# Performance work log

Measured on AMD Instinct MI355X. Metric: run time of the kernel, lower is better.

## Reference

```python
import jax, jax.numpy as jnp
import numpy as np

B, N, E, H = 32, 1024, 1024, 8
D = E // H      # head_dim = 128, att_mid_dim = [128, 64, 128]
MID = 64


def setup_inputs() -> dict:
    key = jax.random.key(0)
    ks = jax.random.split(key, 12)

    def lin(k, out_d, in_d):
        return (jax.random.normal(k, (out_d, in_d), jnp.float32) * 0.02,
                jnp.zeros((out_d,), jnp.float32))

    Wq, bq = lin(ks[0], E, E)
    Wk, bk = lin(ks[1], E, E)
    Wv, bv = lin(ks[2], E, E)
    Wb, bb = lin(ks[3], MID, D)    # attention_basic: Linear(mid[0]=D -> mid[1]=64) + ReLU
    Wl, bl = lin(ks[4], 1, MID)    # attention_last: Linear(64 -> 1)
    Wl2, bl2 = lin(ks[5], D, MID)  # attention_last2: Linear(64 -> D)
    query = jax.random.normal(ks[6], (B, E), jnp.float32)
    k_in = jax.random.normal(ks[7], (B, N, E), jnp.float32)
    value1 = jax.random.normal(ks[8], (B, E), jnp.float32)
    value2 = jax.random.normal(ks[9], (B, N, E), jnp.float32)
    mask = jax.random.randint(ks[10], (B, N), 0, 2, jnp.int32)
    mask = mask.at[:, 0].set(1)  # guarantee at least one valid position per row
    return {"query": query, "key": k_in, "mask": mask, "value1": value1,
            "value2": value2, "Wq": Wq, "bq": bq, "Wk": Wk, "bk": bk,
            "Wv": Wv, "bv": bv, "Wb": Wb, "bb": bb, "Wl": Wl, "bl": bl,
            "Wl2": Wl2, "bl2": bl2}


def reference(query, key, mask, value1, value2, Wq, bq, Wk, bk, Wv, bv,
              Wb, bb, Wl, bl, Wl2, bl2):
    # --- QKV projections (single-query attention) ---
    Q = (query @ Wq.T + bq).reshape(B, 1, H, D).transpose(0, 2, 1, 3)    # [B,H,1,D]
    K = (key @ Wk.T + bk).reshape(B, N, H, D).transpose(0, 2, 1, 3)      # [B,H,N,D]
    V = (key @ Wv.T + bv).reshape(B, N, H, D).transpose(0, 2, 1, 3)      # [B,H,N,D]
    v1 = value1.reshape(B, H, D)                                          # [B,H,D]
    v2 = (value2 @ Wv.T + bv).reshape(B, N, H, D).transpose(0, 2, 1, 3)   # [B,H,N,D]

    scores = jnp.einsum('bhqd,bhkd->bhqk', Q, K) / jnp.sqrt(jnp.float32(D))  # [B,H,1,N]
    attended = jnp.einsum('bhqk,bhkd->bhqd', scores, V)                      # [B,H,1,D]
    attn_map = jnp.broadcast_to(attended, (B, H, N, D))                      # expand(-1,-1,N,-1)

    # --- SCAtt attn_net ---
    h = jax.nn.relu(jnp.einsum('bhnd,md->bhnm', attn_map, Wb) + bb)          # [B,H,N,64]
    mf = mask.astype(h.dtype)                                                # [B,N]
    mext = mf[:, None, :, None]                                              # [B,1,N,1]
    att_map_pool = jnp.sum(h * mext, axis=2) / jnp.sum(mext, axis=2)         # [B,H,64]
    alpha_spatial = (jnp.einsum('bhnm,om->bhno', h, Wl) + bl)[..., 0]        # [B,H,N]
    alpha_channel = jax.nn.sigmoid(att_map_pool @ Wl2.T + bl2)               # [B,H,D]
    alpha_spatial = jnp.where(mf[:, None, :] == 0, jnp.float32(-1e9), alpha_spatial)
    alpha_spatial = jax.nn.softmax(alpha_spatial, axis=-1)                   # [B,H,N]
    v2_att = jnp.einsum('bhn,bhnd->bhd', alpha_spatial, v2)                  # [B,H,D]
    attn = v1 * v2_att * alpha_channel                                       # [B,H,D]
    return attn.reshape(B, H * D)
```

## Files before the change

kernel.cpp:

```cpp
#include <hip/hip_runtime.h>

#define B_  32
#define N_  1024
#define E_  1024
#define H_  8
#define D_  128
#define MID_ 64
#define NT_  16
#define TR_  64
#define NS2_ 16


__global__ __launch_bounds__(256) void k_pre(
        const float* __restrict__ query, const float* __restrict__ Wq,
        const float* __restrict__ bq, const float* __restrict__ Wk,
        const float* __restrict__ bk, float* __restrict__ qk,
        float* __restrict__ qb,
        const float* __restrict__ value2, const int* __restrict__ mask,
        float* __restrict__ P2)
{
    const int t = threadIdx.x;

    __shared__ float Qp[2][D_];
    __shared__ float Qs[D_];
    __shared__ float red[2];
    __shared__ int rows[N_ / NS2_];
    __shared__ int nrows;

    if (blockIdx.x < 256) {
        const int bh = blockIdx.x;
        const int b = bh >> 3, h = bh & 7;

        {
            const int d = t & 127, half = t >> 7;
            const int row = h * D_ + d;
            const float4* wr = (const float4*)(Wq + (size_t)row * E_) + half * 128;
            const float4* qr = (const float4*)(query + (size_t)b * E_) + half * 128;
            float acc = 0.f;
            #pragma unroll 8
            for (int i = 0; i < 128; ++i) {
                float4 w = wr[i], q = qr[i];
                acc += w.x * q.x + w.y * q.y + w.z * q.z + w.w * q.w;
            }
            Qp[half][d] = acc;
        }
        __syncthreads();
        if (t < D_) {
            const int row = h * D_ + t;
            float q = Qp[0][t] + Qp[1][t] + bq[row];
            Qs[t] = q;
            float qp = q * bk[row];
            #pragma unroll
            for (int off = 32; off; off >>= 1) qp += __shfl_down(qp, off);
            if ((t & 63) == 0) red[t >> 6] = qp;
        }
        __syncthreads();
        if (t == 0) qb[bh] = red[0] + red[1];

        const int e0 = t * 4;
        float4 a = make_float4(0.f, 0.f, 0.f, 0.f);
        const float* wkb = Wk + (size_t)(h * D_) * E_ + e0;
        #pragma unroll 8
        for (int d = 0; d < D_; ++d) {
            float Qd = Qs[d];
            float4 w = *(const float4*)(wkb + (size_t)d * E_);
            a.x += Qd * w.x; a.y += Qd * w.y; a.z += Qd * w.z; a.w += Qd * w.w;
        }
        *(float4*)(qk + (size_t)bh * E_ + e0) = a;
    } else {
        const int idx = blockIdx.x - 256;
        const int b = idx & 31, ns = idx >> 5;
        const int e0 = t * 4;
        const int n0 = ns * (N_ / NS2_);

        if (t == 0) nrows = 0;
        __syncthreads();
        if (t < N_ / NS2_) {
            if (mask[b * N_ + n0 + t]) {
                int i2 = atomicAdd(&nrows, 1);
                rows[i2] = t;
            }
        }
        __syncthreads();
        const int nr = nrows;

        float a0 = 0.f, a1 = 0.f, a2 = 0.f, a3 = 0.f;
        const float* vb = value2 + ((size_t)(b * N_ + n0)) * E_ + e0;
        #pragma unroll 4
        for (int i = 0; i < nr; ++i) {
            float4 v = *(const float4*)(vb + (size_t)rows[i] * E_);
            a0 += v.x; a1 += v.y; a2 += v.z; a3 += v.w;
        }
        float* dst = P2 + (size_t)b * E_ + e0;
        atomicAdd(dst + 0, a0); atomicAdd(dst + 1, a1);
        atomicAdd(dst + 2, a2); atomicAdd(dst + 3, a3);
    }
}

__global__ __launch_bounds__(256) void k_scorepool(
        const float* __restrict__ key, const float* __restrict__ qk,
        const float* __restrict__ qb, float* __restrict__ PP,
        float* __restrict__ ssum)
{
    const int tile = blockIdx.x, b = blockIdx.y;
    const int t = threadIdx.x;
    const int c = t & 31, g = t >> 5;

    __shared__ __align__(16) float qks[H_ * E_];
    __shared__ __align__(16) float ssc[TR_][H_];

    {
        const float4* src = (const float4*)(qk + (size_t)b * H_ * E_);
        float4* dst = (float4*)qks;
        #pragma unroll
        for (int k = 0; k < 8; ++k) dst[t + k * 256] = src[t + k * 256];
    }
    __syncthreads();

    const float scale = 0.08838834764831845f;
    const float* keyb = key + ((size_t)b * N_ + (size_t)tile * TR_) * E_;
    const float4* qks4 = (const float4*)qks;
    const float qbv = qb[b * 8 + (c & 7)];

    float acc[H_][8];
    #pragma unroll
    for (int h = 0; h < H_; ++h)
        #pragma unroll
        for (int j = 0; j < 8; ++j) acc[h][j] = 0.f;

    const float4* kr[8];
    #pragma unroll
    for (int j = 0; j < 8; ++j)
        kr[j] = (const float4*)(keyb + (size_t)(g * 8 + j) * E_);

    #pragma unroll 2
    for (int i = 0; i < 8; ++i) {
        float4 kf[8];
        #pragma unroll
        for (int j = 0; j < 8; ++j) kf[j] = kr[j][i * 32 + c];
        #pragma unroll
        for (int h = 0; h < H_; ++h) {
            float4 qf = qks4[h * 256 + i * 32 + c];
            #pragma unroll
            for (int j = 0; j < 8; ++j) {
                acc[h][j] += qf.x * kf[j].x + qf.y * kf[j].y
                           + qf.z * kf[j].z + qf.w * kf[j].w;
            }
        }
    }
    #pragma unroll
    for (int off = 16; off; off >>= 1) {
        #pragma unroll
        for (int h = 0; h < H_; ++h)
            #pragma unroll
            for (int j = 0; j < 8; ++j)
                acc[h][j] += __shfl_xor(acc[h][j], off);
    }
    float tsum = 0.f;
    #pragma unroll
    for (int h = 0; h < H_; ++h) {
        if (c == h) {
            #pragma unroll
            for (int j = 0; j < 8; ++j) {
                float s = (acc[h][j] + qbv) * scale;
                ssc[g * 8 + j][h] = s;
                tsum += s;
            }
        }
    }
    if (c < H_) atomicAdd(&ssum[b * 8 + c], tsum);
    __syncthreads();

    {
        const int e0 = t * 4;
        float pacc[H_][4] = {};
        const float* kb = keyb + e0;
        #pragma unroll 4
        for (int n = 0; n < TR_; ++n) {
            float4 kv = *(const float4*)(kb + (size_t)n * E_);
            float4 s0 = *(const float4*)&ssc[n][0];
            float4 s1 = *(const float4*)&ssc[n][4];
            pacc[0][0] += s0.x * kv.x; pacc[0][1] += s0.x * kv.y;
            pacc[0][2] += s0.x * kv.z; pacc[0][3] += s0.x * kv.w;
            pacc[1][0] += s0.y * kv.x; pacc[1][1] += s0.y * kv.y;
            pacc[1][2] += s0.y * kv.z; pacc[1][3] += s0.y * kv.w;
            pacc[2][0] += s0.z * kv.x; pacc[2][1] += s0.z * kv.y;
            pacc[2][2] += s0.z * kv.z; pacc[2][3] += s0.z * kv.w;
            pacc[3][0] += s0.w * kv.x; pacc[3][1] += s0.w * kv.y;
            pacc[3][2] += s0.w * kv.z; pacc[3][3] += s0.w * kv.w;
            pacc[4][0] += s1.x * kv.x; pacc[4][1] += s1.x * kv.y;
            pacc[4][2] += s1.x * kv.z; pacc[4][3] += s1.x * kv.w;
            pacc[5][0] += s1.y * kv.x; pacc[5][1] += s1.y * kv.y;
            pacc[5][2] += s1.y * kv.z; pacc[5][3] += s1.y * kv.w;
            pacc[6][0] += s1.z * kv.x; pacc[6][1] += s1.z * kv.y;
            pacc[6][2] += s1.z * kv.z; pacc[6][3] += s1.z * kv.w;
            pacc[7][0] += s1.w * kv.x; pacc[7][1] += s1.w * kv.y;
            pacc[7][2] += s1.w * kv.z; pacc[7][3] += s1.w * kv.w;
        }
        #pragma unroll
        for (int h = 0; h < H_; ++h) {
            float* dst = PP + ((size_t)(b * H_) + h) * E_ + e0;
            atomicAdd(dst + 0, pacc[h][0]); atomicAdd(dst + 1, pacc[h][1]);
            atomicAdd(dst + 2, pacc[h][2]); atomicAdd(dst + 3, pacc[h][3]);
        }
    }
}

__global__ __launch_bounds__(256) void k_final(
        const float* __restrict__ PP, const float* __restrict__ P2,
        const float* __restrict__ ssumg, const int* __restrict__ mask,
        const float* __restrict__ Wv, const float* __restrict__ bv,
        const float* __restrict__ Wb, const float* __restrict__ bb,
        const float* __restrict__ Wl2, const float* __restrict__ bl2,
        const float* __restrict__ value1, float* __restrict__ out)
{
    const int bh = blockIdx.x, b = bh >> 3, h = bh & 7;
    const int t = threadIdx.x;
    const int l = t & 63, w = t >> 6;
    const int rg = l >> 4, cl = l & 15;

    __shared__ __align__(16) float pooled[E_];
    __shared__ __align__(16) float pool2[E_];
    __shared__ float attA_s[D_];
    __shared__ float attV_s[D_];
    __shared__ float att[D_];
    __shared__ float hv[MID_];
    __shared__ float red2[4];
    __shared__ float cnt_s;

    {
        const float4* pp = (const float4*)(PP + ((size_t)(b * H_) + h) * E_);
        const float4* p2 = (const float4*)(P2 + (size_t)b * E_);
        ((float4*)pooled)[t] = pp[t];
        ((float4*)pool2)[t]  = p2[t];

        int ci = 0;
        #pragma unroll
        for (int i = 0; i < 4; ++i) ci += mask[b * N_ + t + i * 256];
        float cf = (float)ci;
        #pragma unroll
        for (int off = 32; off; off >>= 1) cf += __shfl_down(cf, off);
        if (l == 0) red2[w] = cf;
    }
    __syncthreads();
    if (t == 0) cnt_s = red2[0] + red2[1] + red2[2] + red2[3];

    const float4* pooled4 = (const float4*)pooled;
    const float4* pool24  = (const float4*)pool2;
    #pragma unroll 2
    for (int pass = 0; pass < 8; ++pass) {
        const int d = pass * 16 + w * 4 + rg;
        const float4* wvr = (const float4*)(Wv + (size_t)(h * D_ + d) * E_);
        float pA = 0.f, pV = 0.f;
        #pragma unroll 4
        for (int i = 0; i < 16; ++i) {
            float4 wv4 = wvr[cl + i * 16];
            float4 pa = pooled4[cl + i * 16];
            float4 pb = pool24[cl + i * 16];
            pA += wv4.x * pa.x + wv4.y * pa.y + wv4.z * pa.z + wv4.w * pa.w;
            pV += wv4.x * pb.x + wv4.y * pb.y + wv4.z * pb.z + wv4.w * pb.w;
        }
        #pragma unroll
        for (int off = 8; off; off >>= 1) {
            pA += __shfl_xor(pA, off);
            pV += __shfl_xor(pV, off);
        }
        if (cl == 0) { attA_s[d] = pA; attV_s[d] = pV; }
    }
    __syncthreads();
    const float cnt = cnt_s;
    const float ss = ssumg[bh];
    if (t < D_) att[t] = attA_s[t] + ss * bv[h * D_ + t];
    __syncthreads();
    if (t < MID_) {
        float a = bb[t];
        #pragma unroll 4
        for (int d2 = 0; d2 < D_; ++d2) a += att[d2] * Wb[t * D_ + d2];
        hv[t] = fmaxf(a, 0.f);
    }
    __syncthreads();
    if (t < D_) {
        float z = bl2[t];
        #pragma unroll
        for (int m = 0; m < MID_; ++m) z += hv[m] * Wl2[t * MID_ + m];
        float alphac = 1.f / (1.f + expf(-z));
        const float bvd = bv[h * D_ + t];
        float v2a = attV_s[t] / cnt + bvd;
        out[(size_t)b * E_ + h * D_ + t] =
            value1[(size_t)b * E_ + h * D_ + t] * v2a * alphac;
    }
}

extern "C" void kernel_launch(void* const* d_in, const int* in_sizes, int n_in,
                              void* d_out, int out_size, void* d_ws, size_t ws_size,
                              hipStream_t stream)
{
    const float* query  = (const float*)d_in[0];
    const float* key    = (const float*)d_in[1];
    const int*   mask   = (const int*)d_in[2];
    const float* value1 = (const float*)d_in[3];
    const float* value2 = (const float*)d_in[4];
    const float* Wq  = (const float*)d_in[5];
    const float* bq  = (const float*)d_in[6];
    const float* Wk  = (const float*)d_in[7];
    const float* bk  = (const float*)d_in[8];
    const float* Wv  = (const float*)d_in[9];
    const float* bv  = (const float*)d_in[10];
    const float* Wb  = (const float*)d_in[11];
    const float* bb  = (const float*)d_in[12];
    const float* Wl2 = (const float*)d_in[15];
    const float* bl2 = (const float*)d_in[16];
    float* out = (float*)d_out;

    char* ws = (char*)d_ws;
    const size_t OFF_P2 = (size_t)B_ * H_ * E_ * 4;
    const size_t OFF_SS = OFF_P2 + (size_t)B_ * E_ * 4;
    const size_t OFF_QB = OFF_SS + 1024;
    const size_t OFF_QK = OFF_QB + 1024;
    float* PP   = (float*)(ws);
    float* P2   = (float*)(ws + OFF_P2);
    float* ssum = (float*)(ws + OFF_SS);
    float* qb   = (float*)(ws + OFF_QB);
    float* qk   = (float*)(ws + OFF_QK);

    hipMemsetAsync(d_ws, 0, OFF_QB, stream);

    hipLaunchKernelGGL(k_pre, dim3(256 + NS2_ * B_), dim3(256), 0, stream,
                       query, Wq, bq, Wk, bk, qk, qb, value2, mask, P2);
    hipLaunchKernelGGL(k_scorepool, dim3(NT_, B_), dim3(256), 0, stream,
                       key, qk, qb, PP, ssum);
    hipLaunchKernelGGL(k_final, dim3(B_ * H_), dim3(256), 0, stream,
                       PP, P2, ssum, mask, Wv, bv, Wb, bb, Wl2, bl2, value1, out);
}
```

Baseline: 427.0 us.

## Split score/pool and Wv projection across more blocks; coalesce Q projection

The Q projection in k_pre now stages the query row in shared memory and uses 16-lane groups with shuffle reductions, so Wq rows are read coalesced. k_scorepool splits the 8 heads into two groups of 4, which doubles the grid and halves per-thread accumulators. The Wv projection moves into a new k_att kernel spread over 4 blocks per (b,h), and a small k_final handles the tail. The aim is more parallelism and occupancy, at the cost of reading key twice and adding one more kernel launch.

New measurement: 443.1 us. 3.8% more time.

```diff
diff --git a/kernel.cpp b/kernel.cpp
--- a/kernel.cpp
+++ b/kernel.cpp
@@ -21,41 +21,48 @@
 {
     const int t = threadIdx.x;
 
-    __shared__ float Qp[2][D_];
+    __shared__ __align__(16) float qsh[E_];
     __shared__ float Qs[D_];
-    __shared__ float red[2];
+    __shared__ float red[4];
     __shared__ int rows[N_ / NS2_];
     __shared__ int nrows;
 
     if (blockIdx.x < 256) {
         const int bh = blockIdx.x;
         const int b = bh >> 3, h = bh & 7;
-
-        {
-            const int d = t & 127, half = t >> 7;
+        const int l = t & 63, w = t >> 6;
+        const int rg = l >> 4, cl = l & 15;
+
+        ((float4*)qsh)[t] = ((const float4*)(query + (size_t)b * E_))[t];
+        __syncthreads();
+
+        const float4* qsh4 = (const float4*)qsh;
+        float qbacc = 0.f;
+        #pragma unroll 2
+        for (int p = 0; p < 8; ++p) {
+            const int d = p * 16 + w * 4 + rg;
             const int row = h * D_ + d;
-            const float4* wr = (const float4*)(Wq + (size_t)row * E_) + half * 128;
-            const float4* qr = (const float4*)(query + (size_t)b * E_) + half * 128;
+            const float4* wr = (const float4*)(Wq + (size_t)row * E_);
             float acc = 0.f;
-            #pragma unroll 8
-            for (int i = 0; i < 128; ++i) {
-                float4 w = wr[i], q = qr[i];
-                acc += w.x * q.x + w.y * q.y + w.z * q.z + w.w * q.w;
-            }
-            Qp[half][d] = acc;
-        }
+            #pragma unroll 4
+            for (int i = 0; i < 16; ++i) {
+                float4 wv = wr[cl + i * 16];
+                float4 qv = qsh4[cl + i * 16];
+                acc += wv.x * qv.x + wv.y * qv.y + wv.z * qv.z + wv.w * qv.w;
+            }
+            #pragma unroll
+            for (int off = 8; off; off >>= 1) acc += __shfl_xor(acc, off);
+            if (cl == 0) {
+                float q = acc + bq[row];
+                Qs[d] = q;
+                qbacc += q * bk[row];
+            }
+        }
+        #pragma unroll
+        for (int off = 32; off; off >>= 1) qbacc += __shfl_down(qbacc, off);
+        if (l == 0) red[w] = qbacc;
         __syncthreads();
-        if (t < D_) {
-            const int row = h * D_ + t;
-            float q = Qp[0][t] + Qp[1][t] + bq[row];
-            Qs[t] = q;
-            float qp = q * bk[row];
-            #pragma unroll
-            for (int off = 32; off; off >>= 1) qp += __shfl_down(qp, off);
-            if ((t & 63) == 0) red[t >> 6] = qp;
-        }
-        __syncthreads();
-        if (t == 0) qb[bh] = red[0] + red[1];
+        if (t == 0) qb[bh] = red[0] + red[1] + red[2] + red[3];
 
         const int e0 = t * 4;
         float4 a = make_float4(0.f, 0.f, 0.f, 0.f);
@@ -63,8 +70,8 @@
         #pragma unroll 8
         for (int d = 0; d < D_; ++d) {
             float Qd = Qs[d];
-            float4 w = *(const float4*)(wkb + (size_t)d * E_);
-            a.x += Qd * w.x; a.y += Qd * w.y; a.z += Qd * w.z; a.w += Qd * w.w;
+            float4 wv = *(const float4*)(wkb + (size_t)d * E_);
+            a.x += Qd * wv.x; a.y += Qd * wv.y; a.z += Qd * wv.z; a.w += Qd * wv.w;
         }
         *(float4*)(qk + (size_t)bh * E_ + e0) = a;
     } else {
@@ -102,31 +109,32 @@
         const float* __restrict__ qb, float* __restrict__ PP,
         float* __restrict__ ssum)
 {
-    const int tile = blockIdx.x, b = blockIdx.y;
+    const int hh = blockIdx.x;
+    const int tile = blockIdx.y, b = blockIdx.z;
     const int t = threadIdx.x;
     const int c = t & 31, g = t >> 5;
 
-    __shared__ __align__(16) float qks[H_ * E_];
-    __shared__ __align__(16) float ssc[TR_][H_];
+    __shared__ __align__(16) float qks[4 * E_];
+    __shared__ __align__(16) float ssc[TR_][4];
 
     {
-        const float4* src = (const float4*)(qk + (size_t)b * H_ * E_);
+        const float4* src = (const float4*)(qk + ((size_t)b * H_ + hh * 4) * E_);
         float4* dst = (float4*)qks;
         #pragma unroll
-        for (int k = 0; k < 8; ++k) dst[t + k * 256] = src[t + k * 256];
+        for (int k = 0; k < 4; ++k) dst[t + k * 256] = src[t + k * 256];
     }
     __syncthreads();
 
     const float scale = 0.08838834764831845f;
     const float* keyb = key + ((size_t)b * N_ + (size_t)tile * TR_) * E_;
     const float4* qks4 = (const float4*)qks;
-    const float qbv = qb[b * 8 + (c & 7)];
-
-    float acc[H_][8];
-    #pragma unroll
-    for (int h = 0; h < H_; ++h)
-        #pragma unroll
-        for (int j = 0; j < 8; ++j) acc[h][j] = 0.f;
+    const float qbv = qb[b * 8 + hh * 4 + (c & 3)];
+
+    float acc[4][8];
+    #pragma unroll
+    for (int lh = 0; lh < 4; ++lh)
+        #pragma unroll
+        for (int j = 0; j < 8; ++j) acc[lh][j] = 0.f;
 
     const float4* kr[8];
     #pragma unroll
@@ -139,117 +147,87 @@
         #pragma unroll
         for (int j = 0; j < 8; ++j) kf[j] = kr[j][i * 32 + c];
         #pragma unroll
-        for (int h = 0; h < H_; ++h) {
-            float4 qf = qks4[h * 256 + i * 32 + c];
+        for (int lh = 0; lh < 4; ++lh) {
+            float4 qf = qks4[lh * 256 + i * 32 + c];
             #pragma unroll
             for (int j = 0; j < 8; ++j) {
-                acc[h][j] += qf.x * kf[j].x + qf.y * kf[j].y
-                           + qf.z * kf[j].z + qf.w * kf[j].w;
+                acc[lh][j] += qf.x * kf[j].x + qf.y * kf[j].y
+                            + qf.z * kf[j].z + qf.w * kf[j].w;
             }
         }
     }
     #pragma unroll
     for (int off = 16; off; off >>= 1) {
         #pragma unroll
-        for (int h = 0; h < H_; ++h)
+        for (int lh = 0; lh < 4; ++lh)
             #pragma unroll
             for (int j = 0; j < 8; ++j)
-                acc[h][j] += __shfl_xor(acc[h][j], off);
+                acc[lh][j] += __shfl_xor(acc[lh][j], off);
     }
     float tsum = 0.f;
     #pragma unroll
-    for (int h = 0; h < H_; ++h) {
-        if (c == h) {
+    for (int lh = 0; lh < 4; ++lh) {
+        if (c == lh) {
             #pragma unroll
             for (int j = 0; j < 8; ++j) {
-                float s = (acc[h][j] + qbv) * scale;
-                ssc[g * 8 + j][h] = s;
+                float s = (acc[lh][j] + qbv) * scale;
+                ssc[g * 8 + j][lh] = s;
                 tsum += s;
             }
         }
     }
-    if (c < H_) atomicAdd(&ssum[b * 8 + c], tsum);
+    if (c < 4) atomicAdd(&ssum[b * 8 + hh * 4 + c], tsum);
     __syncthreads();
 
     {
         const int e0 = t * 4;
-        float pacc[H_][4] = {};
+        float pacc[4][4] = {};
         const float* kb = keyb + e0;
         #pragma unroll 4
         for (int n = 0; n < TR_; ++n) {
             float4 kv = *(const float4*)(kb + (size_t)n * E_);
-            float4 s0 = *(const float4*)&ssc[n][0];
-            float4 s1 = *(const float4*)&ssc[n][4];
-            pacc[0][0] += s0.x * kv.x; pacc[0][1] += s0.x * kv.y;
-            pacc[0][2] += s0.x * kv.z; pacc[0][3] += s0.x * kv.w;
-            pacc[1][0] += s0.y * kv.x; pacc[1][1] += s0.y * kv.y;
-            pacc[1][2] += s0.y * kv.z; pacc[1][3] += s0.y * kv.w;
-            pacc[2][0] += s0.z * kv.x; pacc[2][1] += s0.z * kv.y;
-            pacc[2][2] += s0.z * kv.z; pacc[2][3] += s0.z * kv.w;
-            pacc[3][0] += s0.w * kv.x; pacc[3][1] += s0.w * kv.y;
-            pacc[3][2] += s0.w * kv.z; pacc[3][3] += s0.w * kv.w;
-            pacc[4][0] += s1.x * kv.x; pacc[4][1] += s1.x * kv.y;
-            pacc[4][2] += s1.x * kv.z; pacc[4][3] += s1.x * kv.w;
-            pacc[5][0] += s1.y * kv.x; pacc[5][1] += s1.y * kv.y;
-            pacc[5][2] += s1.y * kv.z; pacc[5][3] += s1.y * kv.w;
-            pacc[6][0] += s1.z * kv.x; pacc[6][1] += s1.z * kv.y;
-            pacc[6][2] += s1.z * kv.z; pacc[6][3] += s1.z * kv.w;
-            pacc[7][0] += s1.w * kv.x; pacc[7][1] += s1.w * kv.y;
-            pacc[7][2] += s1.w * kv.z; pacc[7][3] += s1.w * kv.w;
-        }
-        #pragma unroll
-        for (int h = 0; h < H_; ++h) {
-            float* dst = PP + ((size_t)(b * H_) + h) * E_ + e0;
-            atomicAdd(dst + 0, pacc[h][0]); atomicAdd(dst + 1, pacc[h][1]);
-            atomicAdd(dst + 2, pacc[h][2]); atomicAdd(dst + 3, pacc[h][3]);
-        }
-    }
-}
-
-__global__ __launch_bounds__(256) void k_final(
+            float4 s = *(const float4*)&ssc[n][0];
+            pacc[0][0] += s.x * kv.x; pacc[0][1] += s.x * kv.y;
+            pacc[0][2] += s.x * kv.z; pacc[0][3] += s.x * kv.w;
+            pacc[1][0] += s.y * kv.x; pacc[1][1] += s.y * kv.y;
+            pacc[1][2] += s.y * kv.z; pacc[1][3] += s.y * kv.w;
+            pacc[2][0] += s.z * kv.x; pacc[2][1] += s.z * kv.y;
+            pacc[2][2] += s.z * kv.z; pacc[2][3] += s.z * kv.w;
+            pacc[3][0] += s.w * kv.x; pacc[3][1] += s.w * kv.y;
+            pacc[3][2] += s.w * kv.z; pacc[3][3] += s.w * kv.w;
+        }
+        #pragma unroll
+        for (int lh = 0; lh < 4; ++lh) {
+            float* dst = PP + ((size_t)(b * H_) + hh * 4 + lh) * E_ + e0;
+            atomicAdd(dst + 0, pacc[lh][0]); atomicAdd(dst + 1, pacc[lh][1]);
+            atomicAdd(dst + 2, pacc[lh][2]); atomicAdd(dst + 3, pacc[lh][3]);
+        }
+    }
+}
+
+__global__ __launch_bounds__(256) void k_att(
         const float* __restrict__ PP, const float* __restrict__ P2,
-        const float* __restrict__ ssumg, const int* __restrict__ mask,
-        const float* __restrict__ Wv, const float* __restrict__ bv,
-        const float* __restrict__ Wb, const float* __restrict__ bb,
-        const float* __restrict__ Wl2, const float* __restrict__ bl2,
-        const float* __restrict__ value1, float* __restrict__ out)
-{
-    const int bh = blockIdx.x, b = bh >> 3, h = bh & 7;
+        const float* __restrict__ Wv,
+        float* __restrict__ attA, float* __restrict__ attV)
+{
+    const int dq = blockIdx.x, bh = blockIdx.y;
+    const int b = bh >> 3, h = bh & 7;
     const int t = threadIdx.x;
     const int l = t & 63, w = t >> 6;
     const int rg = l >> 4, cl = l & 15;
 
     __shared__ __align__(16) float pooled[E_];
     __shared__ __align__(16) float pool2[E_];
-    __shared__ float attA_s[D_];
-    __shared__ float attV_s[D_];
-    __shared__ float att[D_];
-    __shared__ float hv[MID_];
-    __shared__ float red2[4];
-    __shared__ float cnt_s;
-
-    {
-        const float4* pp = (const float4*)(PP + ((size_t)(b * H_) + h) * E_);
-        const float4* p2 = (const float4*)(P2 + (size_t)b * E_);
-        ((float4*)pooled)[t] = pp[t];
-        ((float4*)pool2)[t]  = p2[t];
-
-        int ci = 0;
-        #pragma unroll
-        for (int i = 0; i < 4; ++i) ci += mask[b * N_ + t + i * 256];
-        float cf = (float)ci;
-        #pragma unroll
-        for (int off = 32; off; off >>= 1) cf += __shfl_down(cf, off);
-        if (l == 0) red2[w] = cf;
-    }
-    __syncthreads();
-    if (t == 0) cnt_s = red2[0] + red2[1] + red2[2] + red2[3];
+
+    ((float4*)pooled)[t] = ((const float4*)(PP + ((size_t)(b * H_) + h) * E_))[t];
+    ((float4*)pool2)[t]  = ((const float4*)(P2 + (size_t)b * E_))[t];
+    __syncthreads();
 
     const float4* pooled4 = (const float4*)pooled;
     const float4* pool24  = (const float4*)pool2;
-    #pragma unroll 2
-    for (int pass = 0; pass < 8; ++pass) {
-        const int d = pass * 16 + w * 4 + rg;
+    #pragma unroll
+    for (int p = 0; p < 2; ++p) {
+        const int d = dq * 32 + p * 16 + w * 4 + rg;
         const float4* wvr = (const float4*)(Wv + (size_t)(h * D_ + d) * E_);
         float pA = 0.f, pV = 0.f;
         #pragma unroll 4
@@ -265,13 +243,41 @@
             pA += __shfl_xor(pA, off);
             pV += __shfl_xor(pV, off);
         }
-        if (cl == 0) { attA_s[d] = pA; attV_s[d] = pV; }
-    }
-    __syncthreads();
-    const float cnt = cnt_s;
+        if (cl == 0) {
+            attA[(size_t)bh * D_ + d] = pA;
+            attV[(size_t)bh * D_ + d] = pV;
+        }
+    }
+}
+
+__global__ __launch_bounds__(128) void k_final(
+        const float* __restrict__ attA, const float* __restrict__ attV,
+        const float* __restrict__ ssumg, const int* __restrict__ mask,
+        const float* __restrict__ bv, const float* __restrict__ Wb,
+        const float* __restrict__ bb, const float* __restrict__ Wl2,
+        const float* __restrict__ bl2, const float* __restrict__ value1,
+        float* __restrict__ out)
+{
+    const int bh = blockIdx.x, b = bh >> 3, h = bh & 7;
+    const int t = threadIdx.x;
+
+    __shared__ float att[D_];
+    __shared__ float hv[MID_];
+    __shared__ float red2[2];
+    __shared__ float cnt_s;
+
+    int ci = 0;
+    #pragma unroll
+    for (int i = 0; i < 8; ++i) ci += mask[b * N_ + t + i * 128];
+    float cf = (float)ci;
+    #pragma unroll
+    for (int off = 32; off; off >>= 1) cf += __shfl_down(cf, off);
+    if ((t & 63) == 0) red2[t >> 6] = cf;
+
     const float ss = ssumg[bh];
-    if (t < D_) att[t] = attA_s[t] + ss * bv[h * D_ + t];
-    __syncthreads();
+    att[t] = attA[(size_t)bh * D_ + t] + ss * bv[h * D_ + t];
+    __syncthreads();
+    if (t == 0) cnt_s = red2[0] + red2[1];
     if (t < MID_) {
         float a = bb[t];
         #pragma unroll 4
@@ -279,16 +285,15 @@
         hv[t] = fmaxf(a, 0.f);
     }
     __syncthreads();
-    if (t < D_) {
-        float z = bl2[t];
-        #pragma unroll
-        for (int m = 0; m < MID_; ++m) z += hv[m] * Wl2[t * MID_ + m];
-        float alphac = 1.f / (1.f + expf(-z));
-        const float bvd = bv[h * D_ + t];
-        float v2a = attV_s[t] / cnt + bvd;
-        out[(size_t)b * E_ + h * D_ + t] =
-            value1[(size_t)b * E_ + h * D_ + t] * v2a * alphac;
-    }
+
+    float z = bl2[t];
+    #pragma unroll
+    for (int m = 0; m < MID_; ++m) z += hv[m] * Wl2[t * MID_ + m];
+    float alphac = 1.f / (1.f + expf(-z));
+    const float bvd = bv[h * D_ + t];
+    float v2a = attV[(size_t)bh * D_ + t] / cnt_s + bvd;
+    out[(size_t)b * E_ + h * D_ + t] =
+        value1[(size_t)b * E_ + h * D_ + t] * v2a * alphac;
 }
 
 extern "C" void kernel_launch(void* const* d_in, const int* in_sizes, int n_in,
@@ -317,18 +322,24 @@
     const size_t OFF_SS = OFF_P2 + (size_t)B_ * E_ * 4;
     const size_t OFF_QB = OFF_SS + 1024;
     const size_t OFF_QK = OFF_QB + 1024;
+    const size_t OFF_AA = OFF_QK + (size_t)B_ * H_ * E_ * 4;
+    const size_t OFF_AV = OFF_AA + (size_t)B_ * H_ * D_ * 4;
     float* PP   = (float*)(ws);
     float* P2   = (float*)(ws + OFF_P2);
     float* ssum = (float*)(ws + OFF_SS);
     float* qb   = (float*)(ws + OFF_QB);
     float* qk   = (float*)(ws + OFF_QK);
+    float* attA = (float*)(ws + OFF_AA);
+    float* attV = (float*)(ws + OFF_AV);
 
     hipMemsetAsync(d_ws, 0, OFF_QB, stream);
 
     hipLaunchKernelGGL(k_pre, dim3(256 + NS2_ * B_), dim3(256), 0, stream,
                        query, Wq, bq, Wk, bk, qk, qb, value2, mask, P2);
-    hipLaunchKernelGGL(k_scorepool, dim3(NT_, B_), dim3(256), 0, stream,
+    hipLaunchKernelGGL(k_scorepool, dim3(2, NT_, B_), dim3(256), 0, stream,
                        key, qk, qb, PP, ssum);
-    hipLaunchKernelGGL(k_final, dim3(B_ * H_), dim3(256), 0, stream,
-                       PP, P2, ssum, mask, Wv, bv, Wb, bb, Wl2, bl2, value1, out);
-}
+    hipLaunchKernelGGL(k_att, dim3(4, B_ * H_), dim3(256), 0, stream,
+                       PP, P2, Wv, attA, attV);
+    hipLaunchKernelGGL(k_final, dim3(B_ * H_), dim3(128), 0, stream,
+                       attA, attV, ssum, mask, bv, Wb, bb, Wl2, bl2, value1, out);
+}
```
